# Optimization experiments

Hardware: AMD Instinct MI355X
Metric: run time of the kernel (lower is better)

## Reference

```python
import jax, jax.numpy as jnp
import numpy as np

B, N, T, D, E, M = 8, 512, 64, 128, 32, 3


def _norm(v):
    return v / jnp.clip(jnp.linalg.norm(v, axis=-1, keepdims=True), 1e-12)


def setup_inputs() -> dict:
    key = jax.random.key(0)
    ks = jax.random.split(key, 14)
    s = 0.05
    x = jax.random.normal(ks[0], (B, N, T, 1), jnp.float32)
    # set_prior: binarized adjacency + self loops, row-normalized
    a = (jax.random.uniform(ks[1], (N, N)) > 0.95).astype(jnp.float32) + jnp.eye(N, dtype=jnp.float32)
    prior = a / jnp.clip(a.sum(1, keepdims=True), 1e-8)
    # orthogonal queries, as in torch __init__ (QR of zero-padded randn)
    rng = np.random.default_rng(0)
    qs = []
    for _ in range(M):
        pad = np.zeros((D, D), np.float32)
        pad[:E] = rng.standard_normal((E, D)).astype(np.float32) * 0.1
        q, _ = np.linalg.qr(pad)
        qs.append(q[:E])
    return {
        "x": x,
        "prior": prior,
        "proj_W": jax.random.normal(ks[2], (D, 1), jnp.float32) * s,
        "proj_b": jnp.zeros((D,), jnp.float32),
        "W_ih": jax.random.normal(ks[3], (3 * D, D), jnp.float32) * s,
        "W_hh": jax.random.normal(ks[4], (3 * D, D), jnp.float32) * s,
        "b_ih": jnp.zeros((3 * D,), jnp.float32),
        "b_hh": jnp.zeros((3 * D,), jnp.float32),
        "space_W": jax.random.normal(ks[5], (M, D, D), jnp.float32) * s,
        "space_b": jnp.zeros((M, D), jnp.float32),
        "router_W": jax.random.normal(ks[6], (M, 2 * D), jnp.float32) * s,
        "router_b": jnp.zeros((M,), jnp.float32),
        "out_W": jax.random.normal(ks[7], (1, D), jnp.float32) * s,
        "out_b": jnp.zeros((1,), jnp.float32),
        "prior_logit": jnp.array(1.0, jnp.float32),
        "queries": jnp.asarray(np.stack(qs)),  # [M, E, D]
    }


def reference(x, prior, proj_W, proj_b, W_ih, W_hh, b_ih, b_hh,
              space_W, space_b, router_W, router_b, out_W, out_b,
              prior_logit, queries):
    b, n, t, _ = x.shape
    d = proj_b.shape[0]
    m, e, _ = queries.shape
    # proj(x.permute(0,2,1,3)).reshape(B*N, T, D)  (faithful reshape of [B,T,N,D])
    hp = jnp.transpose(x, (0, 2, 1, 3)) @ proj_W.T + proj_b  # [B,T,N,D]
    seq = hp.reshape(b * n, t, d)
    xs = jnp.swapaxes(seq, 0, 1)  # [T, BN, D]

    def gru_step(h, xt):
        gi = xt @ W_ih.T + b_ih
        gh = h @ W_hh.T + b_hh
        ir, iz, i_n = jnp.split(gi, 3, axis=-1)
        hr, hz, h_n = jnp.split(gh, 3, axis=-1)
        r = jax.nn.sigmoid(ir + hr)
        z = jax.nn.sigmoid(iz + hz)
        ng = jnp.tanh(i_n + r * h_n)
        return (1.0 - z) * ng + z * h, None

    h, _ = jax.lax.scan(gru_step, jnp.zeros((b * n, d), x.dtype), xs)
    h = h.reshape(b, n, d)

    stats = jnp.concatenate([h.mean(1), jnp.std(h, axis=1, ddof=1)], axis=-1)  # torch std is unbiased
    probs = jax.nn.softmax(stats @ router_W.T + router_b, axis=-1)  # [B,M]

    z_prior = jnp.einsum('ij,bjd->bid', prior, h)

    hs = _norm(jnp.einsum('bnd,mkd->bmnk', h, space_W) + space_b[None, :, None, :])  # [B,M,N,D]
    q = _norm(queries)  # [M,E,D]
    scores = jnp.einsum('bmnd,med->bmen', hs, q)  # [B,M,E,N] (topk over N axis)
    k = min(n, max(4, int(n * 0.05)))
    vals, idx = jax.lax.top_k(scores, k)  # [B,M,E,k]
    w = jax.nn.softmax(vals / 0.7, axis=-1)
    H = jnp.zeros((b, m, e, n), h.dtype).at[
        jnp.arange(b)[:, None, None, None],
        jnp.arange(m)[None, :, None, None],
        jnp.arange(e)[None, None, :, None],
        idx,
    ].set(w)  # [B,M,E,N], transposed layout of torch's [B,N,E]

    Hmix = jnp.einsum('bmen,bm->ben', H, probs)  # [B,E,N] == torch Hmix^T
    edge = jnp.einsum('ben,bnd->bed', Hmix, h)   # Hmix^T @ h
    z_learn = jnp.einsum('ben,bed->bnd', Hmix, edge)  # Hmix @ edge

    alpha = jax.nn.sigmoid(prior_logit)
    out = (alpha * z_prior + (1.0 - alpha) * z_learn) @ out_W.T + out_b  # [B,N,1]
    return out.squeeze(-1), probs
```

## Files before the change

### kernel.cpp

```cpp
#include <hip/hip_runtime.h>
#include <math.h>

#define OFF_U      0
#define OFF_C      384
#define OFF_QN     768
#define OFF_H      13056
#define OFF_PROBS  537344
#define OFF_HV     537376
#define OFF_SCORES 541472
#define OFF_HMIX   934688
#define OFF_WHI    1066016
#define OFF_WLO    1090592
#define OFF_SHI    1115168
#define OFF_SLO    1139744
#define OFF_STATS  1164320
#define OFF_EV     1229856

typedef short bf16x8 __attribute__((ext_vector_type(8)));
typedef float f32x4 __attribute__((ext_vector_type(4)));

union U8 { unsigned short s[8]; bf16x8 v; uint4 u4; };

__device__ __forceinline__ unsigned short bf16_rtn(float f) {
  unsigned int u = __float_as_uint(f);
  return (unsigned short)((u + 0x7FFFu + ((u >> 16) & 1u)) >> 16);
}
__device__ __forceinline__ float bf16_f(unsigned short h) {
  return __uint_as_float(((unsigned int)h) << 16);
}

__global__ __launch_bounds__(256) void prep_kernel(const float* __restrict__ Wih,
                                                   const float* __restrict__ projW,
                                                   const float* __restrict__ projb,
                                                   const float* __restrict__ bih,
                                                   const float* __restrict__ queries,
                                                   const float* __restrict__ Whh,
                                                   const float* __restrict__ spaceW,
                                                   float* __restrict__ ws) {
  const int bid = blockIdx.x, tid = threadIdx.x;
  const int wave = tid >> 6, lane = tid & 63;
  if (bid < 96) {
    int r = bid * 4 + wave;
    float w0 = Wih[r * 128 + lane], w1 = Wih[r * 128 + 64 + lane];
    float u = w0 * projW[lane] + w1 * projW[64 + lane];
    float c = w0 * projb[lane] + w1 * projb[64 + lane];
    for (int off = 32; off; off >>= 1) {
      u += __shfl_xor(u, off);
      c += __shfl_xor(c, off);
    }
    if (lane == 0) {
      ws[OFF_U + r] = u;
      ws[OFF_C + r] = c + bih[r];
    }
  } else if (bid < 120) {
    int r = (bid - 96) * 4 + wave;
    float v0 = queries[r * 128 + lane], v1 = queries[r * 128 + 64 + lane];
    float ss = v0 * v0 + v1 * v1;
    for (int off = 32; off; off >>= 1) ss += __shfl_xor(ss, off);
    float inv = 1.f / fmaxf(sqrtf(ss), 1e-12f);
    ws[OFF_QN + r * 128 + lane] = v0 * inv;
    ws[OFF_QN + r * 128 + 64 + lane] = v1 * inv;
  } else if (bid < 136) {
    unsigned short* WHI = (unsigned short*)(ws + OFF_WHI);
    unsigned short* WLO = (unsigned short*)(ws + OFF_WLO);
    int base = (bid - 120) * 3072;
    for (int i = tid; i < 3072; i += 256) {
      float w = Whh[base + i];
      unsigned short hi = bf16_rtn(w);
      WHI[base + i] = hi;
      WLO[base + i] = bf16_rtn(w - bf16_f(hi));
    }
  } else if (bid < 152) {
    unsigned short* SHI = (unsigned short*)(ws + OFF_SHI);
    unsigned short* SLO = (unsigned short*)(ws + OFF_SLO);
    int base = (bid - 136) * 3072;
    for (int i = tid; i < 3072; i += 256) {
      float w = spaceW[base + i];
      unsigned short hi = bf16_rtn(w);
      SHI[base + i] = hi;
      SLO[base + i] = bf16_rtn(w - bf16_f(hi));
    }
  } else {
    ws[OFF_EV + tid] = 0.f;
  }
}

__global__ __launch_bounds__(512, 2) void gru_kernel(const float* __restrict__ x,
                                                     const float* __restrict__ bhh,
                                                     const float* __restrict__ outW,
                                                     float* __restrict__ ws) {
  __shared__ __align__(16) unsigned short hB[2][16 * 17 * 8];
  __shared__ float xsAll[16 * 65];
  __shared__ float hFin[16 * 132];

  const int tid = threadIdx.x, wave = tid >> 6, lane = tid & 63;
  const int q = lane >> 4, s15 = lane & 15;
  const int d = wave * 16 + s15;
  const unsigned short* WHI = (const unsigned short*)(ws + OFF_WHI);
  const unsigned short* WLO = (const unsigned short*)(ws + OFF_WLO);

  {
    float4 z4 = make_float4(0.f, 0.f, 0.f, 0.f);
    float4* hm4 = (float4*)(ws + OFF_HMIX);
    if (tid < 128) hm4[blockIdx.x * 128 + tid] = z4;
  }

  bf16x8 Bhi[3][4], Blo[3][4];
#pragma unroll
  for (int t = 0; t < 3; ++t) {
    int row = (wave + 8 * t) * 16 + s15;
#pragma unroll
    for (int c = 0; c < 4; ++c) {
      Bhi[t][c] = *(const bf16x8*)&WHI[row * 128 + c * 32 + q * 8];
      Blo[t][c] = *(const bf16x8*)&WLO[row * 128 + c * 32 + q * 8];
    }
  }
  const float ur = ws[OFF_U + d],       uz = ws[OFF_U + 128 + d], un = ws[OFF_U + 256 + d];
  const float cr = ws[OFF_C + d] + bhh[d];
  const float cz = ws[OFF_C + 128 + d] + bhh[128 + d];
  const float cn = ws[OFF_C + 256 + d];
  const float bj2 = bhh[256 + d];

  const int seq0 = blockIdx.x * 16;
  for (int i = tid; i < 1024; i += 512) {
    int s = i >> 6, tt = i & 63;
    int r = (seq0 + s) * 64 + tt;
    xsAll[s * 65 + tt] = x[((r >> 15) * 512 + (r & 511)) * 64 + ((r >> 9) & 63)];
  }
  for (int i = tid; i < 2176; i += 512) hB[0][i] = 0;
  __syncthreads();

  float hreg[4] = {0.f, 0.f, 0.f, 0.f};
  const int g = d >> 3, e = d & 7;

  for (int t = 0; t < 64; ++t) {
    const int rb = t & 1, wb = rb ^ 1;
    f32x4 acc0 = {0.f, 0.f, 0.f, 0.f};
    f32x4 acc1 = {0.f, 0.f, 0.f, 0.f};
    f32x4 acc2 = {0.f, 0.f, 0.f, 0.f};
#pragma unroll
    for (int c = 0; c < 4; ++c) {
      bf16x8 A = *(const bf16x8*)&hB[rb][((c * 4 + q) * 17 + s15) * 8];
      acc0 = __builtin_amdgcn_mfma_f32_16x16x32_bf16(A, Bhi[0][c], acc0, 0, 0, 0);
      acc1 = __builtin_amdgcn_mfma_f32_16x16x32_bf16(A, Bhi[1][c], acc1, 0, 0, 0);
      acc2 = __builtin_amdgcn_mfma_f32_16x16x32_bf16(A, Bhi[2][c], acc2, 0, 0, 0);
      acc0 = __builtin_amdgcn_mfma_f32_16x16x32_bf16(A, Blo[0][c], acc0, 0, 0, 0);
      acc1 = __builtin_amdgcn_mfma_f32_16x16x32_bf16(A, Blo[1][c], acc1, 0, 0, 0);
      acc2 = __builtin_amdgcn_mfma_f32_16x16x32_bf16(A, Blo[2][c], acc2, 0, 0, 0);
    }
    float xsv[4];
#pragma unroll
    for (int r = 0; r < 4; ++r) xsv[r] = xsAll[(q * 4 + r) * 65 + t];
#pragma unroll
    for (int r = 0; r < 4; ++r) {
      int s = q * 4 + r;
      float gr = fmaf(xsv[r], ur, cr + acc0[r]);
      float gz = fmaf(xsv[r], uz, cz + acc1[r]);
      float gn = fmaf(xsv[r], un, cn);
      float hn = acc2[r] + bj2;
      float rr = __builtin_amdgcn_rcpf(1.f + __expf(-gr));
      float zz = 1.f - __builtin_amdgcn_rcpf(1.f + __expf(-gz));
      float a = fmaf(rr, hn, gn);
      float ng = 1.f - 2.f * __builtin_amdgcn_rcpf(__expf(2.f * a) + 1.f);
      float hv = fmaf(zz, ng - hreg[r], hreg[r]);
      hreg[r] = hv;
      hB[wb][(g * 17 + s) * 8 + e] = bf16_rtn(hv);
    }
    __syncthreads();
  }

#pragma unroll
  for (int r = 0; r < 4; ++r) hFin[(q * 4 + r) * 132 + d] = hreg[r];
  __syncthreads();
  float* h_out = ws + OFF_H;
#pragma unroll
  for (int p = 0; p < 4; ++p) {
    int item = tid + p * 512;
    int s = item >> 7, dd = item & 127;
    h_out[(seq0 + s) * 128 + dd] = hFin[s * 132 + dd];
  }
  for (int s = wave * 2; s < wave * 2 + 2; ++s) {
    float a = hFin[s * 132 + lane] * outW[lane] + hFin[s * 132 + 64 + lane] * outW[64 + lane];
    for (int off = 32; off; off >>= 1) a += __shfl_xor(a, off);
    if (lane == 0) ws[OFF_HV + seq0 + s] = a;
  }
  if (tid < 128) {
    float s = 0.f, q2 = 0.f;
#pragma unroll
    for (int sI = 0; sI < 16; ++sI) {
      float v = hFin[sI * 132 + tid];
      s += v; q2 += v * v;
    }
    ws[OFF_STATS + blockIdx.x * 256 + tid] = s;
    ws[OFF_STATS + blockIdx.x * 256 + 128 + tid] = q2;
  }
}

__global__ __launch_bounds__(256) void scores_kernel(const float* __restrict__ spaceb,
                                                     const float* __restrict__ routerW,
                                                     const float* __restrict__ routerb,
                                                     float* __restrict__ ws,
                                                     float* __restrict__ d_out) {
  const int bid = blockIdx.x;
  const int chunk = bid & 15, m = (bid >> 4) % 3, b = bid / 48;
  const int n0 = chunk * 32;
  const int tid = threadIdx.x, wave = tid >> 6, lane = tid & 63;
  const int q = lane >> 4, s15 = lane & 15;

  __shared__ __align__(16) unsigned short sHi[16 * 33 * 8];
  __shared__ __align__(16) unsigned short sLo[16 * 33 * 8];
  __shared__ float hsL[32 * 132];
  __shared__ float biasL[128];
  __shared__ float invnL[32];

  const float* hG = ws + OFF_H;
  const unsigned short* SHI = (const unsigned short*)(ws + OFF_SHI);
  const unsigned short* SLO = (const unsigned short*)(ws + OFF_SLO);

  if (tid < 128) biasL[tid] = spaceb[m * 128 + tid];
  {
    int nn = tid >> 3, kc = tid & 7;
    const float* row = &hG[(b * 512 + n0 + nn) * 128 + kc * 16];
    U8 ph0, pl0, ph1, pl1;
#pragma unroll
    for (int j = 0; j < 8; ++j) {
      float v = row[j];
      unsigned short hi = bf16_rtn(v);
      ph0.s[j] = hi; pl0.s[j] = bf16_rtn(v - bf16_f(hi));
    }
#pragma unroll
    for (int j = 0; j < 8; ++j) {
      float v = row[8 + j];
      unsigned short hi = bf16_rtn(v);
      ph1.s[j] = hi; pl1.s[j] = bf16_rtn(v - bf16_f(hi));
    }
    int g0 = kc * 2;
    *(uint4*)&sHi[(g0 * 33 + nn) * 8] = ph0.u4;
    *(uint4*)&sLo[(g0 * 33 + nn) * 8] = pl0.u4;
    *(uint4*)&sHi[((g0 + 1) * 33 + nn) * 8] = ph1.u4;
    *(uint4*)&sLo[((g0 + 1) * 33 + nn) * 8] = pl1.u4;
  }
  __syncthreads();

  const int nt = wave >> 1;
  const int dt0 = (wave & 1) * 4;
  f32x4 acc[4] = {{0.f,0.f,0.f,0.f},{0.f,0.f,0.f,0.f},{0.f,0.f,0.f,0.f},{0.f,0.f,0.f,0.f}};
#pragma unroll
  for (int c = 0; c < 4; ++c) {
    bf16x8 Ahi = *(const bf16x8*)&sHi[((c * 4 + q) * 33 + nt * 16 + s15) * 8];
    bf16x8 Alo = *(const bf16x8*)&sLo[((c * 4 + q) * 33 + nt * 16 + s15) * 8];
#pragma unroll
    for (int i = 0; i < 4; ++i) {
      int row = m * 16384 + ((dt0 + i) * 16 + s15) * 128 + c * 32 + q * 8;
      bf16x8 Bhi = *(const bf16x8*)&SHI[row];
      bf16x8 Blo = *(const bf16x8*)&SLO[row];
      acc[i] = __builtin_amdgcn_mfma_f32_16x16x32_bf16(Ahi, Bhi, acc[i], 0, 0, 0);
      acc[i] = __builtin_amdgcn_mfma_f32_16x16x32_bf16(Alo, Bhi, acc[i], 0, 0, 0);
      acc[i] = __builtin_amdgcn_mfma_f32_16x16x32_bf16(Ahi, Blo, acc[i], 0, 0, 0);
    }
  }
#pragma unroll
  for (int i = 0; i < 4; ++i) {
    int dcol = (dt0 + i) * 16 + s15;
    float bb = biasL[dcol];
#pragma unroll
    for (int r = 0; r < 4; ++r)
      hsL[(nt * 16 + q * 4 + r) * 132 + dcol] = acc[i][r] + bb;
  }
  __syncthreads();

  {
    int n = tid >> 3, kc = tid & 7;
    float ss = 0.f;
#pragma unroll
    for (int d4 = 0; d4 < 4; ++d4) {
      float4 v = *(const float4*)&hsL[n * 132 + kc * 16 + d4 * 4];
      ss += v.x * v.x + v.y * v.y + v.z * v.z + v.w * v.w;
    }
    ss += __shfl_xor(ss, 1); ss += __shfl_xor(ss, 2); ss += __shfl_xor(ss, 4);
    if (kc == 0) invnL[n] = 1.f / fmaxf(sqrtf(ss), 1e-12f);
  }
  __syncthreads();

  {
    int n = tid & 31, eg = tid >> 5;
    const float* qn = ws + OFF_QN + (m * 32 + eg * 4) * 128;
    float a0 = 0.f, a1 = 0.f, a2 = 0.f, a3 = 0.f;
#pragma unroll
    for (int d4 = 0; d4 < 32; ++d4) {
      float4 hv = *(const float4*)&hsL[n * 132 + d4 * 4];
      float4 q0 = *(const float4*)&qn[d4 * 4];
      float4 q1 = *(const float4*)&qn[128 + d4 * 4];
      float4 q2 = *(const float4*)&qn[256 + d4 * 4];
      float4 q3 = *(const float4*)&qn[384 + d4 * 4];
      a0 += hv.x * q0.x + hv.y * q0.y + hv.z * q0.z + hv.w * q0.w;
      a1 += hv.x * q1.x + hv.y * q1.y + hv.z * q1.z + hv.w * q1.w;
      a2 += hv.x * q2.x + hv.y * q2.y + hv.z * q2.z + hv.w * q2.w;
      a3 += hv.x * q3.x + hv.y * q3.y + hv.z * q3.z + hv.w * q3.w;
    }
    float inv = invnL[n];
    float* sc = ws + OFF_SCORES + ((b * 3 + m) * 32 + eg * 4) * 512 + n0 + n;
    sc[0]    = a0 * inv;
    sc[512]  = a1 * inv;
    sc[1024] = a2 * inv;
    sc[1536] = a3 * inv;
  }

  if ((bid % 48) == 0) {
    __syncthreads();
    float* st = hsL;
    float* lgS = hsL + 256;
    if (tid < 128) {
      float s = 0.f, q2 = 0.f;
      const float* base = ws + OFF_STATS + b * 32 * 256;
      for (int j = 0; j < 32; ++j) {
        s += base[j * 256 + tid];
        q2 += base[j * 256 + 128 + tid];
      }
      float mean = s * (1.f / 512.f);
      float var = (q2 - 512.f * mean * mean) * (1.f / 511.f);
      st[tid] = mean;
      st[128 + tid] = sqrtf(fmaxf(var, 0.f));
    }
    __syncthreads();
    if (tid < 3) {
      float acc2 = routerb[tid];
      for (int k = 0; k < 256; ++k) acc2 += st[k] * routerW[tid * 256 + k];
      lgS[tid] = acc2;
    }
    __syncthreads();
    if (tid == 0) {
      float mx = fmaxf(lgS[0], fmaxf(lgS[1], lgS[2]));
      float e0 = expf(lgS[0] - mx), e1 = expf(lgS[1] - mx), e2 = expf(lgS[2] - mx);
      float inv = 1.f / (e0 + e1 + e2);
      ws[OFF_PROBS + b * 3 + 0] = e0 * inv;
      ws[OFF_PROBS + b * 3 + 1] = e1 * inv;
      ws[OFF_PROBS + b * 3 + 2] = e2 * inv;
      d_out[4096 + b * 3 + 0] = e0 * inv;
      d_out[4096 + b * 3 + 1] = e1 * inv;
      d_out[4096 + b * 3 + 2] = e2 * inv;
    }
  }
}

__global__ __launch_bounds__(256) void topk_kernel(float* __restrict__ ws) {
  const int row0 = blockIdx.x * 4;
  const int b = row0 / 96;
  const int tid = threadIdx.x, wave = tid >> 6, lane = tid & 63;
  __shared__ float hvL[512];
  hvL[tid] = ws[OFF_HV + b * 512 + tid];
  hvL[256 + tid] = ws[OFF_HV + b * 512 + 256 + tid];
  __syncthreads();

  int row = row0 + wave;
  int m = (row / 32) % 3, e = row & 31;
  const float* sc = ws + OFF_SCORES + row * 512;
  float prob = ws[OFF_PROBS + b * 3 + m];

  float v[8];
#pragma unroll
  for (int j = 0; j < 8; ++j) v[j] = sc[j * 64 + lane];

  float selv = 0.f; int seli = 0; float maxv = 0.f;
  for (int it = 0; it < 25; ++it) {
    float bv = v[0]; int bj = 0;
#pragma unroll
    for (int j = 1; j < 8; ++j)
      if (v[j] > bv) { bv = v[j]; bj = j; }
    int bidx = bj * 64 + lane;
    for (int off = 32; off; off >>= 1) {
      float ov = __shfl_xor(bv, off);
      int oi = __shfl_xor(bidx, off);
      if (ov > bv || (ov == bv && oi < bidx)) { bv = ov; bidx = oi; }
    }
    if (lane == (bidx & 63)) v[bidx >> 6] = -INFINITY;
    if (it == 0) maxv = bv;
    if (lane == it) { selv = bv; seli = bidx; }
  }
  float ex = (lane < 25) ? __expf((selv - maxv) * (1.f / 0.7f)) : 0.f;
  float den = ex;
  for (int off = 32; off; off >>= 1) den += __shfl_xor(den, off);
  float w = prob * ex / den;
  if (lane < 25)
    atomicAdd(&ws[OFF_HMIX + (b * 32 + e) * 512 + seli], w);
  float evc = (lane < 25) ? w * hvL[seli] : 0.f;
  for (int off = 32; off; off >>= 1) evc += __shfl_xor(evc, off);
  if (lane == 0) atomicAdd(&ws[OFF_EV + b * 32 + e], evc);
}

__global__ __launch_bounds__(512) void final_kernel(const float* __restrict__ prior,
                                                    const float* __restrict__ outb,
                                                    const float* __restrict__ plog,
                                                    float* __restrict__ ws,
                                                    float* __restrict__ d_out) {
  const int bid = blockIdx.x;
  const int b = bid >> 4, ch = bid & 15;
  const int tid = threadIdx.x, wave = tid >> 6, lane = tid & 63;
  __shared__ float hvL[512], evL[32];
  hvL[tid] = ws[OFF_HV + b * 512 + tid];
  if (tid < 32) evL[tid] = ws[OFF_EV + b * 32 + tid];
  __syncthreads();
  float alpha = 1.f / (1.f + expf(-plog[0]));
  float ob = outb[0];
#pragma unroll
  for (int i = 0; i < 4; ++i) {
    int n = ch * 32 + wave * 4 + i;
    const float* pr = prior + n * 512;
    float s1 = 0.f;
#pragma unroll
    for (int j = 0; j < 8; ++j) s1 += pr[j * 64 + lane] * hvL[j * 64 + lane];
    float s2 = 0.f;
    if (lane < 32) s2 = ws[OFF_HMIX + (b * 32 + lane) * 512 + n] * evL[lane];
    float a = alpha * s1 + (1.f - alpha) * s2;
    for (int off = 32; off; off >>= 1) a += __shfl_xor(a, off);
    if (lane == 0) d_out[b * 512 + n] = a + ob;
  }
}

extern "C" void kernel_launch(void* const* d_in, const int* in_sizes, int n_in,
                              void* d_out, int out_size, void* d_ws, size_t ws_size,
                              hipStream_t stream) {
  const float* x       = (const float*)d_in[0];
  const float* prior   = (const float*)d_in[1];
  const float* projW   = (const float*)d_in[2];
  const float* projb   = (const float*)d_in[3];
  const float* Wih     = (const float*)d_in[4];
  const float* Whh     = (const float*)d_in[5];
  const float* bih     = (const float*)d_in[6];
  const float* bhh     = (const float*)d_in[7];
  const float* spaceW  = (const float*)d_in[8];
  const float* spaceb  = (const float*)d_in[9];
  const float* routerW = (const float*)d_in[10];
  const float* routerb = (const float*)d_in[11];
  const float* outW    = (const float*)d_in[12];
  const float* outb    = (const float*)d_in[13];
  const float* plog    = (const float*)d_in[14];
  const float* queries = (const float*)d_in[15];
  float* ws  = (float*)d_ws;
  float* out = (float*)d_out;

  prep_kernel<<<153, 256, 0, stream>>>(Wih, projW, projb, bih, queries, Whh, spaceW, ws);
  gru_kernel<<<256, 512, 0, stream>>>(x, bhh, outW, ws);
  scores_kernel<<<384, 256, 0, stream>>>(spaceb, routerW, routerb, ws, out);
  topk_kernel<<<192, 256, 0, stream>>>(ws);
  final_kernel<<<128, 512, 0, stream>>>(prior, outb, plog, ws, out);
}
```

Measured before the change: 192.1 us.

## Fold normalized queries into space weights and compute scores with MFMA

Precomputes Q·W_space and Q·b_space per mixture in the prep kernel, split into bf16 hi/lo pairs. The scores kernel then produces query scores directly with extra MFMA ops on the h tile, scaled by the inverse row norm. This removes the scalar fp32 dot-product loop over the hsL shared tile. The cost is more work in the prep kernel (a serial 128-long loop per thread) and possible rounding differences from the split-bf16 products.

```diff
diff --git a/kernel.cpp b/kernel.cpp
--- a/kernel.cpp
+++ b/kernel.cpp
@@ -3,7 +3,8 @@
 
 #define OFF_U      0
 #define OFF_C      384
-#define OFF_QN     768
+#define OFF_QWHI   768
+#define OFF_QWLO   6912
 #define OFF_H      13056
 #define OFF_PROBS  537344
 #define OFF_HV     537376
@@ -15,6 +16,7 @@
 #define OFF_SLO    1139744
 #define OFF_STATS  1164320
 #define OFF_EV     1229856
+#define OFF_QB     1230112
 
 typedef short bf16x8 __attribute__((ext_vector_type(8)));
 typedef float f32x4 __attribute__((ext_vector_type(4)));
@@ -36,6 +38,7 @@
                                                    const float* __restrict__ queries,
                                                    const float* __restrict__ Whh,
                                                    const float* __restrict__ spaceW,
+                                                   const float* __restrict__ spaceb,
                                                    float* __restrict__ ws) {
   const int bid = blockIdx.x, tid = threadIdx.x;
   const int wave = tid >> 6, lane = tid & 63;
@@ -52,34 +55,55 @@
       ws[OFF_U + r] = u;
       ws[OFF_C + r] = c + bih[r];
     }
-  } else if (bid < 120) {
-    int r = (bid - 96) * 4 + wave;
-    float v0 = queries[r * 128 + lane], v1 = queries[r * 128 + 64 + lane];
-    float ss = v0 * v0 + v1 * v1;
-    for (int off = 32; off; off >>= 1) ss += __shfl_xor(ss, off);
-    float inv = 1.f / fmaxf(sqrtf(ss), 1e-12f);
-    ws[OFF_QN + r * 128 + lane] = v0 * inv;
-    ws[OFF_QN + r * 128 + 64 + lane] = v1 * inv;
-  } else if (bid < 136) {
+  } else if (bid < 112) {
     unsigned short* WHI = (unsigned short*)(ws + OFF_WHI);
     unsigned short* WLO = (unsigned short*)(ws + OFF_WLO);
-    int base = (bid - 120) * 3072;
+    int base = (bid - 96) * 3072;
     for (int i = tid; i < 3072; i += 256) {
       float w = Whh[base + i];
       unsigned short hi = bf16_rtn(w);
       WHI[base + i] = hi;
       WLO[base + i] = bf16_rtn(w - bf16_f(hi));
     }
-  } else if (bid < 152) {
+  } else if (bid < 128) {
     unsigned short* SHI = (unsigned short*)(ws + OFF_SHI);
     unsigned short* SLO = (unsigned short*)(ws + OFF_SLO);
-    int base = (bid - 136) * 3072;
+    int base = (bid - 112) * 3072;
     for (int i = tid; i < 3072; i += 256) {
       float w = spaceW[base + i];
       unsigned short hi = bf16_rtn(w);
       SHI[base + i] = hi;
       SLO[base + i] = bf16_rtn(w - bf16_f(hi));
     }
+  } else if (bid < 224) {
+    int qi = bid - 128;
+    int m = qi >> 5, e = qi & 31;
+    __shared__ float invS, qdS;
+    const float* qrow = queries + (m * 32 + e) * 128;
+    if (wave == 0) {
+      float v0 = qrow[lane], v1 = qrow[64 + lane];
+      float ss = v0 * v0 + v1 * v1;
+      for (int off = 32; off; off >>= 1) ss += __shfl_xor(ss, off);
+      if (lane == 0) invS = 1.f / fmaxf(sqrtf(ss), 1e-12f);
+    } else if (wave == 1) {
+      float v = qrow[lane] * spaceb[m * 128 + lane] +
+                qrow[64 + lane] * spaceb[m * 128 + 64 + lane];
+      for (int off = 32; off; off >>= 1) v += __shfl_xor(v, off);
+      if (lane == 0) qdS = v;
+    }
+    __syncthreads();
+    if (tid < 128) {
+      int din = tid;
+      float acc = 0.f;
+      for (int dout = 0; dout < 128; ++dout)
+        acc += qrow[dout] * spaceW[m * 16384 + dout * 128 + din];
+      acc *= invS;
+      unsigned short hi = bf16_rtn(acc);
+      ((unsigned short*)(ws + OFF_QWHI))[(m * 32 + e) * 128 + din] = hi;
+      ((unsigned short*)(ws + OFF_QWLO))[(m * 32 + e) * 128 + din] =
+          bf16_rtn(acc - bf16_f(hi));
+    }
+    if (tid == 255) ws[OFF_QB + m * 32 + e] = qdS * invS;
   } else {
     ws[OFF_EV + tid] = 0.f;
   }
@@ -212,12 +236,16 @@
   __shared__ float hsL[32 * 132];
   __shared__ float biasL[128];
   __shared__ float invnL[32];
+  __shared__ float qbL[32];
 
   const float* hG = ws + OFF_H;
   const unsigned short* SHI = (const unsigned short*)(ws + OFF_SHI);
   const unsigned short* SLO = (const unsigned short*)(ws + OFF_SLO);
+  const unsigned short* QWHI = (const unsigned short*)(ws + OFF_QWHI);
+  const unsigned short* QWLO = (const unsigned short*)(ws + OFF_QWLO);
 
   if (tid < 128) biasL[tid] = spaceb[m * 128 + tid];
+  else if (tid < 160) qbL[tid - 128] = ws[OFF_QB + m * 32 + (tid - 128)];
   {
     int nn = tid >> 3, kc = tid & 7;
     const float* row = &hG[(b * 512 + n0 + nn) * 128 + kc * 16];
@@ -243,8 +271,10 @@
   __syncthreads();
 
   const int nt = wave >> 1;
-  const int dt0 = (wave & 1) * 4;
+  const int half = wave & 1;
+  const int dt0 = half * 4;
   f32x4 acc[4] = {{0.f,0.f,0.f,0.f},{0.f,0.f,0.f,0.f},{0.f,0.f,0.f,0.f},{0.f,0.f,0.f,0.f}};
+  f32x4 accS = {0.f, 0.f, 0.f, 0.f};
 #pragma unroll
   for (int c = 0; c < 4; ++c) {
     bf16x8 Ahi = *(const bf16x8*)&sHi[((c * 4 + q) * 33 + nt * 16 + s15) * 8];
@@ -258,6 +288,14 @@
       acc[i] = __builtin_amdgcn_mfma_f32_16x16x32_bf16(Alo, Bhi, acc[i], 0, 0, 0);
       acc[i] = __builtin_amdgcn_mfma_f32_16x16x32_bf16(Ahi, Blo, acc[i], 0, 0, 0);
     }
+    {
+      int row = (m * 32 + half * 16 + s15) * 128 + c * 32 + q * 8;
+      bf16x8 Qhi = *(const bf16x8*)&QWHI[row];
+      bf16x8 Qlo = *(const bf16x8*)&QWLO[row];
+      accS = __builtin_amdgcn_mfma_f32_16x16x32_bf16(Ahi, Qhi, accS, 0, 0, 0);
+      accS = __builtin_amdgcn_mfma_f32_16x16x32_bf16(Alo, Qhi, accS, 0, 0, 0);
+      accS = __builtin_amdgcn_mfma_f32_16x16x32_bf16(Ahi, Qlo, accS, 0, 0, 0);
+    }
   }
 #pragma unroll
   for (int i = 0; i < 4; ++i) {
@@ -283,27 +321,15 @@
   __syncthreads();
 
   {
-    int n = tid & 31, eg = tid >> 5;
-    const float* qn = ws + OFF_QN + (m * 32 + eg * 4) * 128;
-    float a0 = 0.f, a1 = 0.f, a2 = 0.f, a3 = 0.f;
-#pragma unroll
-    for (int d4 = 0; d4 < 32; ++d4) {
-      float4 hv = *(const float4*)&hsL[n * 132 + d4 * 4];
-      float4 q0 = *(const float4*)&qn[d4 * 4];
-      float4 q1 = *(const float4*)&qn[128 + d4 * 4];
-      float4 q2 = *(const float4*)&qn[256 + d4 * 4];
-      float4 q3 = *(const float4*)&qn[384 + d4 * 4];
-      a0 += hv.x * q0.x + hv.y * q0.y + hv.z * q0.z + hv.w * q0.w;
-      a1 += hv.x * q1.x + hv.y * q1.y + hv.z * q1.z + hv.w * q1.w;
-      a2 += hv.x * q2.x + hv.y * q2.y + hv.z * q2.z + hv.w * q2.w;
-      a3 += hv.x * q3.x + hv.y * q3.y + hv.z * q3.z + hv.w * q3.w;
-    }
-    float inv = invnL[n];
-    float* sc = ws + OFF_SCORES + ((b * 3 + m) * 32 + eg * 4) * 512 + n0 + n;
-    sc[0]    = a0 * inv;
-    sc[512]  = a1 * inv;
-    sc[1024] = a2 * inv;
-    sc[1536] = a3 * inv;
+    int e = half * 16 + s15;
+    float qb = qbL[e];
+    int nb = nt * 16 + q * 4;
+    float4 o;
+    o.x = (accS[0] + qb) * invnL[nb + 0];
+    o.y = (accS[1] + qb) * invnL[nb + 1];
+    o.z = (accS[2] + qb) * invnL[nb + 2];
+    o.w = (accS[3] + qb) * invnL[nb + 3];
+    *(float4*)&ws[OFF_SCORES + ((b * 3 + m) * 32 + e) * 512 + n0 + nb] = o;
   }
 
   if ((bid % 48) == 0) {
@@ -439,7 +465,8 @@
   float* ws  = (float*)d_ws;
   float* out = (float*)d_out;
 
-  prep_kernel<<<153, 256, 0, stream>>>(Wih, projW, projb, bih, queries, Whh, spaceW, ws);
+  prep_kernel<<<225, 256, 0, stream>>>(Wih, projW, projb, bih, queries, Whh,
+                                       spaceW, spaceb, ws);
   gru_kernel<<<256, 512, 0, stream>>>(x, bhh, outW, ws);
   scores_kernel<<<384, 256, 0, stream>>>(spaceb, routerW, routerb, ws, out);
   topk_kernel<<<192, 256, 0, stream>>>(ws);
```

After: 186.0 us. 3.1% less time.
